# Kernel optimization log

Hardware: AMD Instinct MI355X
Metric: run time of the kernel (lower is better)

## Reference

```python
import jax, jax.numpy as jnp
import numpy as np

MESSAGE_PASSES = 3
HID = 100        # hidden_node_features == message_size
EDGE_F = 4       # n_edge_features
OUT = 100        # readout output dim


def setup_inputs() -> dict:
    key = jax.random.key(0)
    ks = jax.random.split(key, 8)
    B, N = 32, 128
    nodes = jax.random.normal(ks[0], (B, N, HID), dtype=jnp.float32)
    edges = jax.random.uniform(ks[1], (B, N, N, EDGE_F), dtype=jnp.float32)
    s = 1.0 / np.sqrt(HID)
    Wv = jax.random.normal(ks[2], (HID, HID), dtype=jnp.float32) * s
    Ww = jax.random.normal(ks[3], (HID, HID), dtype=jnp.float32) * s
    We = jax.random.normal(ks[4], (EDGE_F, HID), dtype=jnp.float32) * (1.0 / np.sqrt(EDGE_F))
    Wu = jax.random.normal(ks[5], (2 * HID, HID), dtype=jnp.float32) * (1.0 / np.sqrt(2 * HID))
    Wr = jax.random.normal(ks[6], (2 * HID, OUT), dtype=jnp.float32) * (1.0 / np.sqrt(2 * HID))
    return {"nodes": nodes, "edges": edges, "Wv": Wv, "Ww": Ww, "We": We, "Wu": Wu, "Wr": Wr}


def reference(nodes, edges, Wv, Ww, We, Wu, Wr):
    # adjacency[b,v,w] = sum_e edges[b,v,w,e]; nonzero entries define the edge set
    adjacency = edges.sum(axis=-1)                       # [B,N,N]
    edge_mask = adjacency != 0                           # [B,N,N]
    node_mask = adjacency.sum(axis=-1) != 0              # [B,N]

    # edge feature projection is constant across message passes
    e_proj = jnp.einsum('bvwe,eh->bvwh', edges, We)      # [B,N,N,H]

    hidden = nodes                                       # hidden_node_features == node feat dim
    for _ in range(MESSAGE_PASSES):
        # message_terms for every (b, v, w) edge: relu(h_v Wv + h_w Ww + e_vw We)
        pre = (hidden @ Wv)[:, :, None, :] + (hidden @ Ww)[:, None, :, :] + e_proj
        mterms = jnp.where(edge_mask[..., None], jax.nn.relu(pre), 0.0)
        # (same_batch * same_node) matmul == segment-sum over neighbors w
        messages = mterms.sum(axis=2)                    # [B,N,H]
        # update only nodes that appear in the edge set (degree > 0)
        upd = jnp.tanh(jnp.concatenate([hidden, messages], axis=-1) @ Wu)
        hidden = jnp.where(node_mask[..., None], upd, hidden)

    # readout: masked sum-pool of per-node graph terms
    graph_terms = jax.nn.relu(jnp.concatenate([hidden, nodes], axis=-1) @ Wr)  # [B,N,OUT]
    output = jnp.where(node_mask[..., None], graph_terms, 0.0).sum(axis=1)     # [B,OUT]
    return output
```

## Files before the change

### kernel.cpp

```cpp
#include <hip/hip_runtime.h>
#include <math.h>

#define B_   32
#define N_   128
#define H_   100
#define ROWS (B_ * N_)
#define RH   (ROWS * H_)
#define OUTSZ (B_ * H_)

__global__ __launch_bounds__(256, 6) void k_proj0(const float* __restrict__ nodes,
                                                  const float* __restrict__ Ww,
                                                  float* __restrict__ hw,
                                                  float* __restrict__ out) {
    __shared__ float nod_s[2][H_];
    const int row0 = blockIdx.x * 2;
    const int t = threadIdx.x, r = t >> 7, j = t & 127;
    {
        const int gid = blockIdx.x * 256 + t;
        if (gid < OUTSZ) out[gid] = 0.f;
    }
    {
        const float4* ng = (const float4*)(nodes + (size_t)row0 * H_);
        if (t < 50) ((float4*)nod_s)[t] = ng[t];
    }
    __syncthreads();
    if (j >= H_) return;
    const float4* h4p = (const float4*)nod_s[r];
    float wa = 0.f;
#pragma unroll 5
    for (int k4 = 0; k4 < 25; ++k4) {
        const float4 h4 = h4p[k4];
        const int k = k4 * 4;
        wa = fmaf(h4.x, Ww[(k + 0) * H_ + j], wa);
        wa = fmaf(h4.y, Ww[(k + 1) * H_ + j], wa);
        wa = fmaf(h4.z, Ww[(k + 2) * H_ + j], wa);
        wa = fmaf(h4.w, Ww[(k + 3) * H_ + j], wa);
    }
    hw[(size_t)(row0 + r) * H_ + j] = wa;
}

template <int MODE, int INIT_HV>
__global__ __launch_bounds__(256, 6) void k_pass(const float* __restrict__ edges,
                                                 const float* __restrict__ We,
                                                 const float* __restrict__ Wu,
                                                 const float* __restrict__ Wv,
                                                 const float* __restrict__ Ww,
                                                 const float* __restrict__ Wr,
                                                 const float* __restrict__ nodes,
                                                 float* __restrict__ hv_io,
                                                 const float* __restrict__ hw_in,
                                                 float* __restrict__ hw_out,
                                                 const float* __restrict__ hid_in,
                                                 float* __restrict__ hidden,
                                                 float* __restrict__ out) {
    __shared__ float4 e_s[2][N_];
    __shared__ float  asum_part[4];
    __shared__ unsigned qmask_s[2][4];
    __shared__ float  hid_s[2][H_];
    __shared__ float  msg_s[2][H_];
    __shared__ float  hn_s[2][H_];
    __shared__ float  nod_s[2][H_];
    __shared__ float  red_s[2][H_];

    const int bx = blockIdx.x;
    const int cu = bx & 255, slot = bx >> 8;
    const int b = cu >> 3;
    const int vt = (cu & 7) + slot * 8;
    const int row0 = b * N_ + vt * 2;

    const int t = threadIdx.x, r = t >> 7, j = t & 127;
    const int wv = t >> 6, lane = t & 63;
    const int row = row0 + r;
    const bool act = (j < H_);

    {
        const float4* eg = (const float4*)(edges + (size_t)row0 * N_ * 4);
        const float4 e = eg[t];
        e_s[r][j] = e;
        float s = (e.x + e.y) + (e.z + e.w);
        const unsigned long long bal = __ballot(s != 0.f);
        if (lane == 0) {
            qmask_s[wv >> 1][(wv & 1) * 2]     = (unsigned)bal;
            qmask_s[wv >> 1][(wv & 1) * 2 + 1] = (unsigned)(bal >> 32);
        }
#pragma unroll
        for (int off = 32; off > 0; off >>= 1) s += __shfl_down(s, off);
        if (lane == 0) asum_part[wv] = s;
    }
    {
        const float4* hg = (const float4*)(hid_in + (size_t)row0 * H_);
        if (t < 50) ((float4*)hid_s)[t] = hg[t];
        if (MODE == 2) {
            const float4* ng = (const float4*)(nodes + (size_t)row0 * H_);
            if (t < 50) ((float4*)nod_s)[t] = ng[t];
        }
    }
    __syncthreads();

    const float nm = ((asum_part[2 * r] + asum_part[2 * r + 1]) != 0.f) ? 1.f : 0.f;

    if (act) {
        float hvv;
        if (INIT_HV) {
            const float4* h4p = (const float4*)hid_s[r];
            float va = 0.f;
#pragma unroll 5
            for (int k4 = 0; k4 < 25; ++k4) {
                const float4 h4 = h4p[k4];
                const int k = k4 * 4;
                va = fmaf(h4.x, Wv[(k + 0) * H_ + j], va);
                va = fmaf(h4.y, Wv[(k + 1) * H_ + j], va);
                va = fmaf(h4.z, Wv[(k + 2) * H_ + j], va);
                va = fmaf(h4.w, Wv[(k + 3) * H_ + j], va);
            }
            hvv = va;
        } else {
            hvv = hv_io[(size_t)row * H_ + j];
        }
        const float we0 = We[0 * H_ + j], we1 = We[1 * H_ + j];
        const float we2 = We[2 * H_ + j], we3 = We[3 * H_ + j];
        const float* hwp = hw_in + (size_t)b * N_ * H_ + j;
        float acc = 0.f;
        for (int c = 0; c < 4; ++c) {
            const unsigned mq =
                __builtin_amdgcn_readfirstlane(qmask_s[r][c]);
            const float4* ec = &e_s[r][c * 32];
            const float*  hc = hwp + (size_t)(c * 32) * H_;
#pragma unroll 8
            for (int w8 = 0; w8 < 32; ++w8) {
                const float4 e = ec[w8];
                const float  hww = hc[w8 * H_];
                const float  m = ((mq >> w8) & 1u) ? 1.f : 0.f;
                float p = hvv + hww;
                p = fmaf(e.x, we0, p);
                p = fmaf(e.y, we1, p);
                p = fmaf(e.z, we2, p);
                p = fmaf(e.w, we3, p);
                acc = fmaf(m, fmaxf(p, 0.f), acc);
            }
        }
        msg_s[r][j] = acc;
    }
    __syncthreads();

    if (act) {
        const float4* h4p = (const float4*)hid_s[r];
        const float4* m4p = (const float4*)msg_s[r];
        float u = 0.f;
#pragma unroll 5
        for (int k4 = 0; k4 < 25; ++k4) {
            const float4 h4 = h4p[k4];
            const int k = k4 * 4;
            u = fmaf(h4.x, Wu[(k + 0) * H_ + j], u);
            u = fmaf(h4.y, Wu[(k + 1) * H_ + j], u);
            u = fmaf(h4.z, Wu[(k + 2) * H_ + j], u);
            u = fmaf(h4.w, Wu[(k + 3) * H_ + j], u);
        }
#pragma unroll 5
        for (int k4 = 0; k4 < 25; ++k4) {
            const float4 m4 = m4p[k4];
            const int k = H_ + k4 * 4;
            u = fmaf(m4.x, Wu[(k + 0) * H_ + j], u);
            u = fmaf(m4.y, Wu[(k + 1) * H_ + j], u);
            u = fmaf(m4.z, Wu[(k + 2) * H_ + j], u);
            u = fmaf(m4.w, Wu[(k + 3) * H_ + j], u);
        }
        const float nh = (nm != 0.f) ? tanhf(u) : hid_s[r][j];
        hn_s[r][j] = nh;
        if (MODE == 1) hidden[(size_t)row * H_ + j] = nh;
    }
    __syncthreads();

    if (MODE == 1) {
        if (act) {
            const float4* h4p = (const float4*)hn_s[r];
            float va = 0.f, wa = 0.f;
#pragma unroll 5
            for (int k4 = 0; k4 < 25; ++k4) {
                const float4 h4 = h4p[k4];
                const int k = k4 * 4;
                va = fmaf(h4.x, Wv[(k + 0) * H_ + j], va);
                wa = fmaf(h4.x, Ww[(k + 0) * H_ + j], wa);
                va = fmaf(h4.y, Wv[(k + 1) * H_ + j], va);
                wa = fmaf(h4.y, Ww[(k + 1) * H_ + j], wa);
                va = fmaf(h4.z, Wv[(k + 2) * H_ + j], va);
                wa = fmaf(h4.z, Ww[(k + 2) * H_ + j], wa);
                va = fmaf(h4.w, Wv[(k + 3) * H_ + j], va);
                wa = fmaf(h4.w, Ww[(k + 3) * H_ + j], wa);
            }
            hv_io[(size_t)row * H_ + j] = va;
            hw_out[(size_t)row * H_ + j] = wa;
        }
    } else {
        if (act) {
            const float4* h4p = (const float4*)hn_s[r];
            const float4* n4p = (const float4*)nod_s[r];
            float u = 0.f;
#pragma unroll 5
            for (int k4 = 0; k4 < 25; ++k4) {
                const float4 h4 = h4p[k4];
                const int k = k4 * 4;
                u = fmaf(h4.x, Wr[(k + 0) * H_ + j], u);
                u = fmaf(h4.y, Wr[(k + 1) * H_ + j], u);
                u = fmaf(h4.z, Wr[(k + 2) * H_ + j], u);
                u = fmaf(h4.w, Wr[(k + 3) * H_ + j], u);
            }
#pragma unroll 5
            for (int k4 = 0; k4 < 25; ++k4) {
                const float4 n4 = n4p[k4];
                const int k = H_ + k4 * 4;
                u = fmaf(n4.x, Wr[(k + 0) * H_ + j], u);
                u = fmaf(n4.y, Wr[(k + 1) * H_ + j], u);
                u = fmaf(n4.z, Wr[(k + 2) * H_ + j], u);
                u = fmaf(n4.w, Wr[(k + 3) * H_ + j], u);
            }
            red_s[r][j] = nm * fmaxf(u, 0.f);
        }
        __syncthreads();
        if (t < H_) atomicAdd(out + b * H_ + t, red_s[0][t] + red_s[1][t]);
    }
}

extern "C" void kernel_launch(void* const* d_in, const int* in_sizes, int n_in,
                              void* d_out, int out_size, void* d_ws, size_t ws_size,
                              hipStream_t stream) {
    const float* nodes = (const float*)d_in[0];
    const float* edges = (const float*)d_in[1];
    const float* Wv    = (const float*)d_in[2];
    const float* Ww    = (const float*)d_in[3];
    const float* We    = (const float*)d_in[4];
    const float* Wu    = (const float*)d_in[5];
    const float* Wr    = (const float*)d_in[6];
    float* out = (float*)d_out;

    float* hidden = (float*)d_ws;
    float* hv     = hidden + RH;
    float* hwA    = hv + RH;
    float* hwB    = hwA + RH;

    k_proj0<<<ROWS / 2, 256, 0, stream>>>(nodes, Ww, hwA, out);

    k_pass<1, 1><<<ROWS / 2, 256, 0, stream>>>(edges, We, Wu, Wv, Ww, Wr, nodes,
                                               hv, hwA, hwB, nodes, hidden, out);
    k_pass<1, 0><<<ROWS / 2, 256, 0, stream>>>(edges, We, Wu, Wv, Ww, Wr, nodes,
                                               hv, hwB, hwA, hidden, hidden, out);
    k_pass<2, 0><<<ROWS / 2, 256, 0, stream>>>(edges, We, Wu, Wv, Ww, Wr, nodes,
                                               hv, hwA, hwB, hidden, hidden, out);
}
```

Before: 198.9 us.

## Register-block four rows per thread to reuse weight and neighbor loads

```diff
diff --git a/kernel.cpp b/kernel.cpp
--- a/kernel.cpp
+++ b/kernel.cpp
@@ -7,40 +7,51 @@
 #define ROWS (B_ * N_)
 #define RH   (ROWS * H_)
 #define OUTSZ (B_ * H_)
-
-__global__ __launch_bounds__(256, 6) void k_proj0(const float* __restrict__ nodes,
+#define RPB  8
+#define RPT  4
+
+__global__ __launch_bounds__(256, 2) void k_proj0(const float* __restrict__ nodes,
                                                   const float* __restrict__ Ww,
                                                   float* __restrict__ hw,
                                                   float* __restrict__ out) {
-    __shared__ float nod_s[2][H_];
-    const int row0 = blockIdx.x * 2;
-    const int t = threadIdx.x, r = t >> 7, j = t & 127;
+    __shared__ float nod_s[RPB][H_];
+    const int bx = blockIdx.x;
+    const int row0 = bx * RPB;
+    const int t = threadIdx.x, rg = t >> 7, j = t & 127;
     {
-        const int gid = blockIdx.x * 256 + t;
+        const int gid = bx * 256 + t;
         if (gid < OUTSZ) out[gid] = 0.f;
     }
     {
         const float4* ng = (const float4*)(nodes + (size_t)row0 * H_);
-        if (t < 50) ((float4*)nod_s)[t] = ng[t];
+        if (t < 200) ((float4*)nod_s)[t] = ng[t];
     }
     __syncthreads();
     if (j >= H_) return;
-    const float4* h4p = (const float4*)nod_s[r];
-    float wa = 0.f;
+    float wa[RPT] = {0.f, 0.f, 0.f, 0.f};
 #pragma unroll 5
     for (int k4 = 0; k4 < 25; ++k4) {
-        const float4 h4 = h4p[k4];
         const int k = k4 * 4;
-        wa = fmaf(h4.x, Ww[(k + 0) * H_ + j], wa);
-        wa = fmaf(h4.y, Ww[(k + 1) * H_ + j], wa);
-        wa = fmaf(h4.z, Ww[(k + 2) * H_ + j], wa);
-        wa = fmaf(h4.w, Ww[(k + 3) * H_ + j], wa);
-    }
-    hw[(size_t)(row0 + r) * H_ + j] = wa;
+        const float w0 = Ww[(k + 0) * H_ + j];
+        const float w1 = Ww[(k + 1) * H_ + j];
+        const float w2 = Ww[(k + 2) * H_ + j];
+        const float w3 = Ww[(k + 3) * H_ + j];
+#pragma unroll
+        for (int r = 0; r < RPT; ++r) {
+            const float4 h4 = ((const float4*)nod_s[rg * RPT + r])[k4];
+            wa[r] = fmaf(h4.x, w0, wa[r]);
+            wa[r] = fmaf(h4.y, w1, wa[r]);
+            wa[r] = fmaf(h4.z, w2, wa[r]);
+            wa[r] = fmaf(h4.w, w3, wa[r]);
+        }
+    }
+#pragma unroll
+    for (int r = 0; r < RPT; ++r)
+        hw[(size_t)(row0 + rg * RPT + r) * H_ + j] = wa[r];
 }
 
 template <int MODE, int INIT_HV>
-__global__ __launch_bounds__(256, 6) void k_pass(const float* __restrict__ edges,
+__global__ __launch_bounds__(256, 2) void k_pass(const float* __restrict__ edges,
                                                  const float* __restrict__ We,
                                                  const float* __restrict__ Wu,
                                                  const float* __restrict__ Wv,
@@ -53,171 +64,242 @@
                                                  const float* __restrict__ hid_in,
                                                  float* __restrict__ hidden,
                                                  float* __restrict__ out) {
-    __shared__ float4 e_s[2][N_];
-    __shared__ float  asum_part[4];
-    __shared__ unsigned qmask_s[2][4];
-    __shared__ float  hid_s[2][H_];
-    __shared__ float  msg_s[2][H_];
-    __shared__ float  hn_s[2][H_];
-    __shared__ float  nod_s[2][H_];
-    __shared__ float  red_s[2][H_];
+    __shared__ float4 e_s[RPB][N_];
+    __shared__ float  asum_s[RPB][2];
+    __shared__ unsigned qmask_s[RPB][4];
+    __shared__ float  hid_s[RPB][H_];
+    __shared__ float  msg_s[RPB][H_];
+    __shared__ float  hn_s[RPB][H_];
+    __shared__ float  nod_s[RPB][H_];
+    __shared__ float  red_s[RPB][H_];
 
     const int bx = blockIdx.x;
-    const int cu = bx & 255, slot = bx >> 8;
-    const int b = cu >> 3;
-    const int vt = (cu & 7) + slot * 8;
-    const int row0 = b * N_ + vt * 2;
-
-    const int t = threadIdx.x, r = t >> 7, j = t & 127;
+    const int b = bx >> 4;
+    const int vt = bx & 15;
+    const int row0 = b * N_ + vt * RPB;
+
+    const int t = threadIdx.x, rg = t >> 7, j = t & 127;
     const int wv = t >> 6, lane = t & 63;
-    const int row = row0 + r;
     const bool act = (j < H_);
 
     {
         const float4* eg = (const float4*)(edges + (size_t)row0 * N_ * 4);
-        const float4 e = eg[t];
-        e_s[r][j] = e;
-        float s = (e.x + e.y) + (e.z + e.w);
-        const unsigned long long bal = __ballot(s != 0.f);
-        if (lane == 0) {
-            qmask_s[wv >> 1][(wv & 1) * 2]     = (unsigned)bal;
-            qmask_s[wv >> 1][(wv & 1) * 2 + 1] = (unsigned)(bal >> 32);
-        }
-#pragma unroll
-        for (int off = 32; off > 0; off >>= 1) s += __shfl_down(s, off);
-        if (lane == 0) asum_part[wv] = s;
+        float4* es = &e_s[0][0];
+#pragma unroll
+        for (int q = 0; q < 4; ++q) {
+            const int idx = q * 256 + t;
+            const float4 e = eg[idx];
+            es[idx] = e;
+            float s = (e.x + e.y) + (e.z + e.w);
+            const unsigned long long bal = __ballot(s != 0.f);
+            const int seg = q * 4 + wv;
+            const int rowq = seg >> 1, half = seg & 1;
+            if (lane == 0) {
+                qmask_s[rowq][half * 2]     = (unsigned)bal;
+                qmask_s[rowq][half * 2 + 1] = (unsigned)(bal >> 32);
+            }
+#pragma unroll
+            for (int off = 32; off > 0; off >>= 1) s += __shfl_down(s, off);
+            if (lane == 0) asum_s[rowq][half] = s;
+        }
     }
     {
         const float4* hg = (const float4*)(hid_in + (size_t)row0 * H_);
-        if (t < 50) ((float4*)hid_s)[t] = hg[t];
+        if (t < 200) ((float4*)hid_s)[t] = hg[t];
         if (MODE == 2) {
             const float4* ng = (const float4*)(nodes + (size_t)row0 * H_);
-            if (t < 50) ((float4*)nod_s)[t] = ng[t];
+            if (t < 200) ((float4*)nod_s)[t] = ng[t];
         }
     }
     __syncthreads();
 
-    const float nm = ((asum_part[2 * r] + asum_part[2 * r + 1]) != 0.f) ? 1.f : 0.f;
+    float nm[RPT];
+#pragma unroll
+    for (int r = 0; r < RPT; ++r) {
+        const int row = rg * RPT + r;
+        nm[r] = ((asum_s[row][0] + asum_s[row][1]) != 0.f) ? 1.f : 0.f;
+    }
 
     if (act) {
-        float hvv;
+        float hv[RPT];
         if (INIT_HV) {
-            const float4* h4p = (const float4*)hid_s[r];
-            float va = 0.f;
+            float va[RPT] = {0.f, 0.f, 0.f, 0.f};
 #pragma unroll 5
             for (int k4 = 0; k4 < 25; ++k4) {
-                const float4 h4 = h4p[k4];
                 const int k = k4 * 4;
-                va = fmaf(h4.x, Wv[(k + 0) * H_ + j], va);
-                va = fmaf(h4.y, Wv[(k + 1) * H_ + j], va);
-                va = fmaf(h4.z, Wv[(k + 2) * H_ + j], va);
-                va = fmaf(h4.w, Wv[(k + 3) * H_ + j], va);
-            }
-            hvv = va;
+                const float w0 = Wv[(k + 0) * H_ + j];
+                const float w1 = Wv[(k + 1) * H_ + j];
+                const float w2 = Wv[(k + 2) * H_ + j];
+                const float w3 = Wv[(k + 3) * H_ + j];
+#pragma unroll
+                for (int r = 0; r < RPT; ++r) {
+                    const float4 h4 = ((const float4*)hid_s[rg * RPT + r])[k4];
+                    va[r] = fmaf(h4.x, w0, va[r]);
+                    va[r] = fmaf(h4.y, w1, va[r]);
+                    va[r] = fmaf(h4.z, w2, va[r]);
+                    va[r] = fmaf(h4.w, w3, va[r]);
+                }
+            }
+#pragma unroll
+            for (int r = 0; r < RPT; ++r) hv[r] = va[r];
         } else {
-            hvv = hv_io[(size_t)row * H_ + j];
+#pragma unroll
+            for (int r = 0; r < RPT; ++r)
+                hv[r] = hv_io[(size_t)(row0 + rg * RPT + r) * H_ + j];
         }
         const float we0 = We[0 * H_ + j], we1 = We[1 * H_ + j];
         const float we2 = We[2 * H_ + j], we3 = We[3 * H_ + j];
         const float* hwp = hw_in + (size_t)b * N_ * H_ + j;
-        float acc = 0.f;
+        float acc[RPT] = {0.f, 0.f, 0.f, 0.f};
         for (int c = 0; c < 4; ++c) {
-            const unsigned mq =
-                __builtin_amdgcn_readfirstlane(qmask_s[r][c]);
-            const float4* ec = &e_s[r][c * 32];
-            const float*  hc = hwp + (size_t)(c * 32) * H_;
+            unsigned mq[RPT];
+#pragma unroll
+            for (int r = 0; r < RPT; ++r)
+                mq[r] = __builtin_amdgcn_readfirstlane(qmask_s[rg * RPT + r][c]);
+            const float* hc = hwp + (size_t)(c * 32) * H_;
 #pragma unroll 8
             for (int w8 = 0; w8 < 32; ++w8) {
-                const float4 e = ec[w8];
-                const float  hww = hc[w8 * H_];
-                const float  m = ((mq >> w8) & 1u) ? 1.f : 0.f;
-                float p = hvv + hww;
-                p = fmaf(e.x, we0, p);
-                p = fmaf(e.y, we1, p);
-                p = fmaf(e.z, we2, p);
-                p = fmaf(e.w, we3, p);
-                acc = fmaf(m, fmaxf(p, 0.f), acc);
-            }
-        }
-        msg_s[r][j] = acc;
+                const float hww = hc[w8 * H_];
+#pragma unroll
+                for (int r = 0; r < RPT; ++r) {
+                    const float4 e = e_s[rg * RPT + r][c * 32 + w8];
+                    float p = hv[r] + hww;
+                    p = fmaf(e.x, we0, p);
+                    p = fmaf(e.y, we1, p);
+                    p = fmaf(e.z, we2, p);
+                    p = fmaf(e.w, we3, p);
+                    const float m = ((mq[r] >> w8) & 1u) ? 1.f : 0.f;
+                    acc[r] = fmaf(m, fmaxf(p, 0.f), acc[r]);
+                }
+            }
+        }
+#pragma unroll
+        for (int r = 0; r < RPT; ++r) msg_s[rg * RPT + r][j] = acc[r];
     }
     __syncthreads();
 
+    float nh[RPT];
     if (act) {
-        const float4* h4p = (const float4*)hid_s[r];
-        const float4* m4p = (const float4*)msg_s[r];
-        float u = 0.f;
+        float u[RPT] = {0.f, 0.f, 0.f, 0.f};
 #pragma unroll 5
         for (int k4 = 0; k4 < 25; ++k4) {
-            const float4 h4 = h4p[k4];
             const int k = k4 * 4;
-            u = fmaf(h4.x, Wu[(k + 0) * H_ + j], u);
-            u = fmaf(h4.y, Wu[(k + 1) * H_ + j], u);
-            u = fmaf(h4.z, Wu[(k + 2) * H_ + j], u);
-            u = fmaf(h4.w, Wu[(k + 3) * H_ + j], u);
+            const float w0 = Wu[(k + 0) * H_ + j];
+            const float w1 = Wu[(k + 1) * H_ + j];
+            const float w2 = Wu[(k + 2) * H_ + j];
+            const float w3 = Wu[(k + 3) * H_ + j];
+#pragma unroll
+            for (int r = 0; r < RPT; ++r) {
+                const float4 h4 = ((const float4*)hid_s[rg * RPT + r])[k4];
+                u[r] = fmaf(h4.x, w0, u[r]);
+                u[r] = fmaf(h4.y, w1, u[r]);
+                u[r] = fmaf(h4.z, w2, u[r]);
+                u[r] = fmaf(h4.w, w3, u[r]);
+            }
         }
 #pragma unroll 5
         for (int k4 = 0; k4 < 25; ++k4) {
-            const float4 m4 = m4p[k4];
             const int k = H_ + k4 * 4;
-            u = fmaf(m4.x, Wu[(k + 0) * H_ + j], u);
-            u = fmaf(m4.y, Wu[(k + 1) * H_ + j], u);
-            u = fmaf(m4.z, Wu[(k + 2) * H_ + j], u);
-            u = fmaf(m4.w, Wu[(k + 3) * H_ + j], u);
-        }
-        const float nh = (nm != 0.f) ? tanhf(u) : hid_s[r][j];
-        hn_s[r][j] = nh;
-        if (MODE == 1) hidden[(size_t)row * H_ + j] = nh;
+            const float w0 = Wu[(k + 0) * H_ + j];
+            const float w1 = Wu[(k + 1) * H_ + j];
+            const float w2 = Wu[(k + 2) * H_ + j];
+            const float w3 = Wu[(k + 3) * H_ + j];
+#pragma unroll
+            for (int r = 0; r < RPT; ++r) {
+                const float4 m4 = ((const float4*)msg_s[rg * RPT + r])[k4];
+                u[r] = fmaf(m4.x, w0, u[r]);
+                u[r] = fmaf(m4.y, w1, u[r]);
+                u[r] = fmaf(m4.z, w2, u[r]);
+                u[r] = fmaf(m4.w, w3, u[r]);
+            }
+        }
+#pragma unroll
+        for (int r = 0; r < RPT; ++r) {
+            const int row = rg * RPT + r;
+            nh[r] = (nm[r] != 0.f) ? tanhf(u[r]) : hid_s[row][j];
+            hn_s[row][j] = nh[r];
+            if (MODE == 1) hidden[(size_t)(row0 + row) * H_ + j] = nh[r];
+        }
     }
     __syncthreads();
 
     if (MODE == 1) {
         if (act) {
-            const float4* h4p = (const float4*)hn_s[r];
-            float va = 0.f, wa = 0.f;
+            float va[RPT] = {0.f, 0.f, 0.f, 0.f};
+            float wa[RPT] = {0.f, 0.f, 0.f, 0.f};
 #pragma unroll 5
             for (int k4 = 0; k4 < 25; ++k4) {
-                const float4 h4 = h4p[k4];
                 const int k = k4 * 4;
-                va = fmaf(h4.x, Wv[(k + 0) * H_ + j], va);
-                wa = fmaf(h4.x, Ww[(k + 0) * H_ + j], wa);
-                va = fmaf(h4.y, Wv[(k + 1) * H_ + j], va);
-                wa = fmaf(h4.y, Ww[(k + 1) * H_ + j], wa);
-                va = fmaf(h4.z, Wv[(k + 2) * H_ + j], va);
-                wa = fmaf(h4.z, Ww[(k + 2) * H_ + j], wa);
-                va = fmaf(h4.w, Wv[(k + 3) * H_ + j], va);
-                wa = fmaf(h4.w, Ww[(k + 3) * H_ + j], wa);
-            }
-            hv_io[(size_t)row * H_ + j] = va;
-            hw_out[(size_t)row * H_ + j] = wa;
+                const float v0 = Wv[(k + 0) * H_ + j], q0 = Ww[(k + 0) * H_ + j];
+                const float v1 = Wv[(k + 1) * H_ + j], q1 = Ww[(k + 1) * H_ + j];
+                const float v2 = Wv[(k + 2) * H_ + j], q2 = Ww[(k + 2) * H_ + j];
+                const float v3 = Wv[(k + 3) * H_ + j], q3 = Ww[(k + 3) * H_ + j];
+#pragma unroll
+                for (int r = 0; r < RPT; ++r) {
+                    const float4 h4 = ((const float4*)hn_s[rg * RPT + r])[k4];
+                    va[r] = fmaf(h4.x, v0, va[r]);
+                    wa[r] = fmaf(h4.x, q0, wa[r]);
+                    va[r] = fmaf(h4.y, v1, va[r]);
+                    wa[r] = fmaf(h4.y, q1, wa[r]);
+                    va[r] = fmaf(h4.z, v2, va[r]);
+                    wa[r] = fmaf(h4.z, q2, wa[r]);
+                    va[r] = fmaf(h4.w, v3, va[r]);
+                    wa[r] = fmaf(h4.w, q3, wa[r]);
+                }
+            }
+#pragma unroll
+            for (int r = 0; r < RPT; ++r) {
+                const size_t g = (size_t)(row0 + rg * RPT + r) * H_ + j;
+                hv_io[g] = va[r];
+                hw_out[g] = wa[r];
+            }
         }
     } else {
         if (act) {
-            const float4* h4p = (const float4*)hn_s[r];
-            const float4* n4p = (const float4*)nod_s[r];
-            float u = 0.f;
+            float u[RPT] = {0.f, 0.f, 0.f, 0.f};
 #pragma unroll 5
             for (int k4 = 0; k4 < 25; ++k4) {
-                const float4 h4 = h4p[k4];
                 const int k = k4 * 4;
-                u = fmaf(h4.x, Wr[(k + 0) * H_ + j], u);
-                u = fmaf(h4.y, Wr[(k + 1) * H_ + j], u);
-                u = fmaf(h4.z, Wr[(k + 2) * H_ + j], u);
-                u = fmaf(h4.w, Wr[(k + 3) * H_ + j], u);
+                const float w0 = Wr[(k + 0) * H_ + j];
+                const float w1 = Wr[(k + 1) * H_ + j];
+                const float w2 = Wr[(k + 2) * H_ + j];
+                const float w3 = Wr[(k + 3) * H_ + j];
+#pragma unroll
+                for (int r = 0; r < RPT; ++r) {
+                    const float4 h4 = ((const float4*)hn_s[rg * RPT + r])[k4];
+                    u[r] = fmaf(h4.x, w0, u[r]);
+                    u[r] = fmaf(h4.y, w1, u[r]);
+                    u[r] = fmaf(h4.z, w2, u[r]);
+                    u[r] = fmaf(h4.w, w3, u[r]);
+                }
             }
 #pragma unroll 5
             for (int k4 = 0; k4 < 25; ++k4) {
-                const float4 n4 = n4p[k4];
                 const int k = H_ + k4 * 4;
-                u = fmaf(n4.x, Wr[(k + 0) * H_ + j], u);
-                u = fmaf(n4.y, Wr[(k + 1) * H_ + j], u);
-                u = fmaf(n4.z, Wr[(k + 2) * H_ + j], u);
-                u = fmaf(n4.w, Wr[(k + 3) * H_ + j], u);
-            }
-            red_s[r][j] = nm * fmaxf(u, 0.f);
+                const float w0 = Wr[(k + 0) * H_ + j];
+                const float w1 = Wr[(k + 1) * H_ + j];
+                const float w2 = Wr[(k + 2) * H_ + j];
+                const float w3 = Wr[(k + 3) * H_ + j];
+#pragma unroll
+                for (int r = 0; r < RPT; ++r) {
+                    const float4 n4 = ((const float4*)nod_s[rg * RPT + r])[k4];
+                    u[r] = fmaf(n4.x, w0, u[r]);
+                    u[r] = fmaf(n4.y, w1, u[r]);
+                    u[r] = fmaf(n4.z, w2, u[r]);
+                    u[r] = fmaf(n4.w, w3, u[r]);
+                }
+            }
+#pragma unroll
+            for (int r = 0; r < RPT; ++r)
+                red_s[rg * RPT + r][j] = nm[r] * fmaxf(u[r], 0.f);
         }
         __syncthreads();
-        if (t < H_) atomicAdd(out + b * H_ + t, red_s[0][t] + red_s[1][t]);
+        if (t < H_) {
+            float ssum = 0.f;
+#pragma unroll
+            for (int rr = 0; rr < RPB; ++rr) ssum += red_s[rr][t];
+            atomicAdd(out + b * H_ + t, ssum);
+        }
     }
 }
 
@@ -238,12 +320,12 @@
     float* hwA    = hv + RH;
     float* hwB    = hwA + RH;
 
-    k_proj0<<<ROWS / 2, 256, 0, stream>>>(nodes, Ww, hwA, out);
-
-    k_pass<1, 1><<<ROWS / 2, 256, 0, stream>>>(edges, We, Wu, Wv, Ww, Wr, nodes,
-                                               hv, hwA, hwB, nodes, hidden, out);
-    k_pass<1, 0><<<ROWS / 2, 256, 0, stream>>>(edges, We, Wu, Wv, Ww, Wr, nodes,
-                                               hv, hwB, hwA, hidden, hidden, out);
-    k_pass<2, 0><<<ROWS / 2, 256, 0, stream>>>(edges, We, Wu, Wv, Ww, Wr, nodes,
-                                               hv, hwA, hwB, hidden, hidden, out);
+    k_proj0<<<ROWS / RPB, 256, 0, stream>>>(nodes, Ww, hwA, out);
+
+    k_pass<1, 1><<<ROWS / RPB, 256, 0, stream>>>(edges, We, Wu, Wv, Ww, Wr, nodes,
+                                                 hv, hwA, hwB, nodes, hidden, out);
+    k_pass<1, 0><<<ROWS / RPB, 256, 0, stream>>>(edges, We, Wu, Wv, Ww, Wr, nodes,
+                                                 hv, hwB, hwA, hidden, hidden, out);
+    k_pass<2, 0><<<ROWS / RPB, 256, 0, stream>>>(edges, We, Wu, Wv, Ww, Wr, nodes,
+                                                 hv, hwA, hwB, hidden, hidden, out);
 }
```

Result: slower. 239.3 us (+20.3%).

## Stage dense weight matrices through double-buffered shared memory chunks

Applied to the files above, without the earlier changes.

```diff
diff --git a/kernel.cpp b/kernel.cpp
--- a/kernel.cpp
+++ b/kernel.cpp
@@ -7,6 +7,8 @@
 #define ROWS (B_ * N_)
 #define RH   (ROWS * H_)
 #define OUTSZ (B_ * H_)
+#define CK   20
+#define CK4  (CK * H_ / 4)
 
 __global__ __launch_bounds__(256, 6) void k_proj0(const float* __restrict__ nodes,
                                                   const float* __restrict__ Ww,
@@ -39,8 +41,15 @@
     hw[(size_t)(row0 + r) * H_ + j] = wa;
 }
 
+__device__ __forceinline__ void stage_chunk(float4* dst, const float* W,
+                                            int k0, int t) {
+    const float4* src = (const float4*)(W + (size_t)k0 * H_);
+    dst[t] = src[t];
+    if (t < CK4 - 256) dst[256 + t] = src[256 + t];
+}
+
 template <int MODE, int INIT_HV>
-__global__ __launch_bounds__(256, 6) void k_pass(const float* __restrict__ edges,
+__global__ __launch_bounds__(256, 7) void k_pass(const float* __restrict__ edges,
                                                  const float* __restrict__ We,
                                                  const float* __restrict__ Wu,
                                                  const float* __restrict__ Wv,
@@ -59,8 +68,8 @@
     __shared__ float  hid_s[2][H_];
     __shared__ float  msg_s[2][H_];
     __shared__ float  hn_s[2][H_];
-    __shared__ float  nod_s[2][H_];
-    __shared__ float  red_s[2][H_];
+    __shared__ float  nod_s[MODE == 2 ? 2 : 1][MODE == 2 ? H_ : 1];
+    __shared__ float4 w4_s[2][CK4];
 
     const int bx = blockIdx.x;
     const int cu = bx & 255, slot = bx >> 8;
@@ -95,6 +104,7 @@
             if (t < 50) ((float4*)nod_s)[t] = ng[t];
         }
     }
+    stage_chunk(w4_s[0], Wu, 0, t);
     __syncthreads();
 
     const float nm = ((asum_part[2 * r] + asum_part[2 * r + 1]) != 0.f) ? 1.f : 0.f;
@@ -143,81 +153,104 @@
     }
     __syncthreads();
 
+    int cur = 0;
+    float u0 = 0.f, u1 = 0.f;
+    for (int c = 0; c < 10; ++c) {
+        if (c < 9)       stage_chunk(w4_s[cur ^ 1], Wu, (c + 1) * CK, t);
+        else if (MODE == 1) stage_chunk(w4_s[cur ^ 1], Wv, 0, t);
+        else             stage_chunk(w4_s[cur ^ 1], Wr, 0, t);
+        if (act) {
+            const float* wb = (const float*)w4_s[cur] + j;
+            const float4* hb = (c < 5) ? ((const float4*)hid_s[r]) + c * 5
+                                       : ((const float4*)msg_s[r]) + (c - 5) * 5;
+#pragma unroll
+            for (int k4 = 0; k4 < 5; ++k4) {
+                const float4 h4 = hb[k4];
+                const float* wr_ = wb + k4 * 4 * H_;
+                u0 = fmaf(h4.x, wr_[0 * H_], u0);
+                u1 = fmaf(h4.y, wr_[1 * H_], u1);
+                u0 = fmaf(h4.z, wr_[2 * H_], u0);
+                u1 = fmaf(h4.w, wr_[3 * H_], u1);
+            }
+        }
+        __syncthreads();
+        cur ^= 1;
+    }
+
     if (act) {
-        const float4* h4p = (const float4*)hid_s[r];
-        const float4* m4p = (const float4*)msg_s[r];
-        float u = 0.f;
-#pragma unroll 5
-        for (int k4 = 0; k4 < 25; ++k4) {
-            const float4 h4 = h4p[k4];
-            const int k = k4 * 4;
-            u = fmaf(h4.x, Wu[(k + 0) * H_ + j], u);
-            u = fmaf(h4.y, Wu[(k + 1) * H_ + j], u);
-            u = fmaf(h4.z, Wu[(k + 2) * H_ + j], u);
-            u = fmaf(h4.w, Wu[(k + 3) * H_ + j], u);
-        }
-#pragma unroll 5
-        for (int k4 = 0; k4 < 25; ++k4) {
-            const float4 m4 = m4p[k4];
-            const int k = H_ + k4 * 4;
-            u = fmaf(m4.x, Wu[(k + 0) * H_ + j], u);
-            u = fmaf(m4.y, Wu[(k + 1) * H_ + j], u);
-            u = fmaf(m4.z, Wu[(k + 2) * H_ + j], u);
-            u = fmaf(m4.w, Wu[(k + 3) * H_ + j], u);
-        }
-        const float nh = (nm != 0.f) ? tanhf(u) : hid_s[r][j];
+        const float nh = (nm != 0.f) ? tanhf(u0 + u1) : hid_s[r][j];
         hn_s[r][j] = nh;
         if (MODE == 1) hidden[(size_t)row * H_ + j] = nh;
     }
     __syncthreads();
 
     if (MODE == 1) {
-        if (act) {
-            const float4* h4p = (const float4*)hn_s[r];
-            float va = 0.f, wa = 0.f;
-#pragma unroll 5
-            for (int k4 = 0; k4 < 25; ++k4) {
-                const float4 h4 = h4p[k4];
-                const int k = k4 * 4;
-                va = fmaf(h4.x, Wv[(k + 0) * H_ + j], va);
-                wa = fmaf(h4.x, Ww[(k + 0) * H_ + j], wa);
-                va = fmaf(h4.y, Wv[(k + 1) * H_ + j], va);
-                wa = fmaf(h4.y, Ww[(k + 1) * H_ + j], wa);
-                va = fmaf(h4.z, Wv[(k + 2) * H_ + j], va);
-                wa = fmaf(h4.z, Ww[(k + 2) * H_ + j], wa);
-                va = fmaf(h4.w, Wv[(k + 3) * H_ + j], va);
-                wa = fmaf(h4.w, Ww[(k + 3) * H_ + j], wa);
-            }
-            hv_io[(size_t)row * H_ + j] = va;
-            hw_out[(size_t)row * H_ + j] = wa;
-        }
+        float a0 = 0.f, a1 = 0.f;
+        for (int c = 0; c < 5; ++c) {
+            if (c < 4) stage_chunk(w4_s[cur ^ 1], Wv, (c + 1) * CK, t);
+            else       stage_chunk(w4_s[cur ^ 1], Ww, 0, t);
+            if (act) {
+                const float* wb = (const float*)w4_s[cur] + j;
+                const float4* hb = ((const float4*)hn_s[r]) + c * 5;
+#pragma unroll
+                for (int k4 = 0; k4 < 5; ++k4) {
+                    const float4 h4 = hb[k4];
+                    const float* wr_ = wb + k4 * 4 * H_;
+                    a0 = fmaf(h4.x, wr_[0 * H_], a0);
+                    a1 = fmaf(h4.y, wr_[1 * H_], a1);
+                    a0 = fmaf(h4.z, wr_[2 * H_], a0);
+                    a1 = fmaf(h4.w, wr_[3 * H_], a1);
+                }
+            }
+            __syncthreads();
+            cur ^= 1;
+        }
+        if (act) hv_io[(size_t)row * H_ + j] = a0 + a1;
+        float b0 = 0.f, b1 = 0.f;
+        for (int c = 0; c < 5; ++c) {
+            if (c < 4) stage_chunk(w4_s[cur ^ 1], Ww, (c + 1) * CK, t);
+            if (act) {
+                const float* wb = (const float*)w4_s[cur] + j;
+                const float4* hb = ((const float4*)hn_s[r]) + c * 5;
+#pragma unroll
+                for (int k4 = 0; k4 < 5; ++k4) {
+                    const float4 h4 = hb[k4];
+                    const float* wr_ = wb + k4 * 4 * H_;
+                    b0 = fmaf(h4.x, wr_[0 * H_], b0);
+                    b1 = fmaf(h4.y, wr_[1 * H_], b1);
+                    b0 = fmaf(h4.z, wr_[2 * H_], b0);
+                    b1 = fmaf(h4.w, wr_[3 * H_], b1);
+                }
+            }
+            if (c < 4) __syncthreads();
+            cur ^= 1;
+        }
+        if (act) hw_out[(size_t)row * H_ + j] = b0 + b1;
     } else {
-        if (act) {
-            const float4* h4p = (const float4*)hn_s[r];
-            const float4* n4p = (const float4*)nod_s[r];
-            float u = 0.f;
-#pragma unroll 5
-            for (int k4 = 0; k4 < 25; ++k4) {
-                const float4 h4 = h4p[k4];
-                const int k = k4 * 4;
-                u = fmaf(h4.x, Wr[(k + 0) * H_ + j], u);
-                u = fmaf(h4.y, Wr[(k + 1) * H_ + j], u);
-                u = fmaf(h4.z, Wr[(k + 2) * H_ + j], u);
-                u = fmaf(h4.w, Wr[(k + 3) * H_ + j], u);
-            }
-#pragma unroll 5
-            for (int k4 = 0; k4 < 25; ++k4) {
-                const float4 n4 = n4p[k4];
-                const int k = H_ + k4 * 4;
-                u = fmaf(n4.x, Wr[(k + 0) * H_ + j], u);
-                u = fmaf(n4.y, Wr[(k + 1) * H_ + j], u);
-                u = fmaf(n4.z, Wr[(k + 2) * H_ + j], u);
-                u = fmaf(n4.w, Wr[(k + 3) * H_ + j], u);
-            }
-            red_s[r][j] = nm * fmaxf(u, 0.f);
-        }
+        float a0 = 0.f, a1 = 0.f;
+        for (int c = 0; c < 10; ++c) {
+            if (c < 9) stage_chunk(w4_s[cur ^ 1], Wr, (c + 1) * CK, t);
+            if (act) {
+                const float* wb = (const float*)w4_s[cur] + j;
+                const float4* hb = (c < 5) ? ((const float4*)hn_s[r]) + c * 5
+                                           : ((const float4*)nod_s[r]) + (c - 5) * 5;
+#pragma unroll
+                for (int k4 = 0; k4 < 5; ++k4) {
+                    const float4 h4 = hb[k4];
+                    const float* wr_ = wb + k4 * 4 * H_;
+                    a0 = fmaf(h4.x, wr_[0 * H_], a0);
+                    a1 = fmaf(h4.y, wr_[1 * H_], a1);
+                    a0 = fmaf(h4.z, wr_[2 * H_], a0);
+                    a1 = fmaf(h4.w, wr_[3 * H_], a1);
+                }
+            }
+            __syncthreads();
+            cur ^= 1;
+        }
+        float* red = (float*)w4_s[0];
+        if (act) red[r * H_ + j] = nm * fmaxf(a0 + a1, 0.f);
         __syncthreads();
-        if (t < H_) atomicAdd(out + b * H_ + t, red_s[0][t] + red_s[1][t]);
+        if (t < H_) atomicAdd(out + b * H_ + t, red[0 * H_ + t] + red[1 * H_ + t]);
     }
 }
 
```

Result: slower. 214.1 us (+7.7%).

## Stage per-graph hw tile in LDS and process eight rows per block

Applied to the files above, without the earlier changes.

```diff
diff --git a/kernel.cpp b/kernel.cpp
--- a/kernel.cpp
+++ b/kernel.cpp
@@ -7,6 +7,7 @@
 #define ROWS (B_ * N_)
 #define RH   (ROWS * H_)
 #define OUTSZ (B_ * H_)
+#define RPB  8
 
 __global__ __launch_bounds__(256, 6) void k_proj0(const float* __restrict__ nodes,
                                                   const float* __restrict__ Ww,
@@ -40,69 +41,74 @@
 }
 
 template <int MODE, int INIT_HV>
-__global__ __launch_bounds__(256, 6) void k_pass(const float* __restrict__ edges,
-                                                 const float* __restrict__ We,
-                                                 const float* __restrict__ Wu,
-                                                 const float* __restrict__ Wv,
-                                                 const float* __restrict__ Ww,
-                                                 const float* __restrict__ Wr,
-                                                 const float* __restrict__ nodes,
-                                                 float* __restrict__ hv_io,
-                                                 const float* __restrict__ hw_in,
-                                                 float* __restrict__ hw_out,
-                                                 const float* __restrict__ hid_in,
-                                                 float* __restrict__ hidden,
-                                                 float* __restrict__ out) {
-    __shared__ float4 e_s[2][N_];
-    __shared__ float  asum_part[4];
-    __shared__ unsigned qmask_s[2][4];
-    __shared__ float  hid_s[2][H_];
-    __shared__ float  msg_s[2][H_];
-    __shared__ float  hn_s[2][H_];
-    __shared__ float  nod_s[2][H_];
-    __shared__ float  red_s[2][H_];
+__global__ __launch_bounds__(1024, 8) void k_pass(const float* __restrict__ edges,
+                                                  const float* __restrict__ We,
+                                                  const float* __restrict__ Wu,
+                                                  const float* __restrict__ Wv,
+                                                  const float* __restrict__ Ww,
+                                                  const float* __restrict__ Wr,
+                                                  const float* __restrict__ nodes,
+                                                  float* __restrict__ hv_io,
+                                                  const float* __restrict__ hw_in,
+                                                  float* __restrict__ hw_out,
+                                                  const float* __restrict__ hid_in,
+                                                  float* __restrict__ hidden,
+                                                  float* __restrict__ out) {
+    __shared__ float  hw_s[N_ * H_];
+    __shared__ float4 e_s[RPB * N_];
+    __shared__ float  asum_s[RPB][2];
+    __shared__ unsigned qmask_s[RPB][4];
+    __shared__ float  hid_s[RPB][H_];
+    __shared__ float  msg_s[RPB][H_];
+    __shared__ float  hn_s[RPB][H_];
 
     const int bx = blockIdx.x;
     const int cu = bx & 255, slot = bx >> 8;
     const int b = cu >> 3;
     const int vt = (cu & 7) + slot * 8;
-    const int row0 = b * N_ + vt * 2;
-
-    const int t = threadIdx.x, r = t >> 7, j = t & 127;
+    const int row0 = b * N_ + vt * RPB;
+
+    const int t = threadIdx.x;
+    const int rg = t >> 7, j = t & 127;
     const int wv = t >> 6, lane = t & 63;
-    const int row = row0 + r;
+    const int row = row0 + rg;
     const bool act = (j < H_);
 
+    {
+        const float4* src = (const float4*)(hw_in + (size_t)b * N_ * H_);
+        float4* dst = (float4*)hw_s;
+        dst[t] = src[t];
+        dst[1024 + t] = src[1024 + t];
+        dst[2048 + t] = src[2048 + t];
+        if (t < 128) dst[3072 + t] = src[3072 + t];
+    }
     {
         const float4* eg = (const float4*)(edges + (size_t)row0 * N_ * 4);
         const float4 e = eg[t];
-        e_s[r][j] = e;
+        e_s[t] = e;
         float s = (e.x + e.y) + (e.z + e.w);
         const unsigned long long bal = __ballot(s != 0.f);
+        const int rowq = wv >> 1, half = wv & 1;
         if (lane == 0) {
-            qmask_s[wv >> 1][(wv & 1) * 2]     = (unsigned)bal;
-            qmask_s[wv >> 1][(wv & 1) * 2 + 1] = (unsigned)(bal >> 32);
+            qmask_s[rowq][half * 2]     = (unsigned)bal;
+            qmask_s[rowq][half * 2 + 1] = (unsigned)(bal >> 32);
         }
 #pragma unroll
         for (int off = 32; off > 0; off >>= 1) s += __shfl_down(s, off);
-        if (lane == 0) asum_part[wv] = s;
+        if (lane == 0) asum_s[rowq][half] = s;
     }
     {
         const float4* hg = (const float4*)(hid_in + (size_t)row0 * H_);
-        if (t < 50) ((float4*)hid_s)[t] = hg[t];
-        if (MODE == 2) {
-            const float4* ng = (const float4*)(nodes + (size_t)row0 * H_);
-            if (t < 50) ((float4*)nod_s)[t] = ng[t];
-        }
-    }
-    __syncthreads();
-
-    const float nm = ((asum_part[2 * r] + asum_part[2 * r + 1]) != 0.f) ? 1.f : 0.f;
+        if (t < 200) ((float4*)hid_s)[t] = hg[t];
+    }
+    __syncthreads();
+
+    const float nm = ((asum_s[rg][0] + asum_s[rg][1]) != 0.f) ? 1.f : 0.f;
 
     if (act) {
         float hvv;
         if (INIT_HV) {
-            const float4* h4p = (const float4*)hid_s[r];
+            const float4* h4p = (const float4*)hid_s[rg];
             float va = 0.f;
 #pragma unroll 5
             for (int k4 = 0; k4 < 25; ++k4) {
@@ -119,12 +125,12 @@
         }
         const float we0 = We[0 * H_ + j], we1 = We[1 * H_ + j];
         const float we2 = We[2 * H_ + j], we3 = We[3 * H_ + j];
-        const float* hwp = hw_in + (size_t)b * N_ * H_ + j;
+        const float* hwp = hw_s + j;
         float acc = 0.f;
         for (int c = 0; c < 4; ++c) {
             const unsigned mq =
-                __builtin_amdgcn_readfirstlane(qmask_s[r][c]);
-            const float4* ec = &e_s[r][c * 32];
+                __builtin_amdgcn_readfirstlane(qmask_s[rg][c]);
+            const float4* ec = &e_s[rg * N_ + c * 32];
             const float*  hc = hwp + (size_t)(c * 32) * H_;
 #pragma unroll 8
             for (int w8 = 0; w8 < 32; ++w8) {
@@ -139,13 +145,19 @@
                 acc = fmaf(m, fmaxf(p, 0.f), acc);
             }
         }
-        msg_s[r][j] = acc;
-    }
-    __syncthreads();
+        msg_s[rg][j] = acc;
+    }
+    __syncthreads();
+
+    if (MODE == 2) {
+        float* nodf = (float*)e_s + 1024;
+        const float4* ng = (const float4*)(nodes + (size_t)row0 * H_);
+        if (t < 200) ((float4*)nodf)[t] = ng[t];
+    }
 
     if (act) {
-        const float4* h4p = (const float4*)hid_s[r];
-        const float4* m4p = (const float4*)msg_s[r];
+        const float4* h4p = (const float4*)hid_s[rg];
+        const float4* m4p = (const float4*)msg_s[rg];
         float u = 0.f;
 #pragma unroll 5
         for (int k4 = 0; k4 < 25; ++k4) {
@@ -165,15 +177,15 @@
             u = fmaf(m4.z, Wu[(k + 2) * H_ + j], u);
             u = fmaf(m4.w, Wu[(k + 3) * H_ + j], u);
         }
-        const float nh = (nm != 0.f) ? tanhf(u) : hid_s[r][j];
-        hn_s[r][j] = nh;
+        const float nh = (nm != 0.f) ? tanhf(u) : hid_s[rg][j];
+        hn_s[rg][j] = nh;
         if (MODE == 1) hidden[(size_t)row * H_ + j] = nh;
     }
     __syncthreads();
 
     if (MODE == 1) {
         if (act) {
-            const float4* h4p = (const float4*)hn_s[r];
+            const float4* h4p = (const float4*)hn_s[rg];
             float va = 0.f, wa = 0.f;
 #pragma unroll 5
             for (int k4 = 0; k4 < 25; ++k4) {
@@ -192,9 +204,11 @@
             hw_out[(size_t)row * H_ + j] = wa;
         }
     } else {
+        float* nodf = (float*)e_s + 1024;
+        float* redf = (float*)e_s;
         if (act) {
-            const float4* h4p = (const float4*)hn_s[r];
-            const float4* n4p = (const float4*)nod_s[r];
+            const float4* h4p = (const float4*)hn_s[rg];
+            const float4* n4p = (const float4*)(nodf + rg * H_);
             float u = 0.f;
 #pragma unroll 5
             for (int k4 = 0; k4 < 25; ++k4) {
@@ -214,10 +228,15 @@
                 u = fmaf(n4.z, Wr[(k + 2) * H_ + j], u);
                 u = fmaf(n4.w, Wr[(k + 3) * H_ + j], u);
             }
-            red_s[r][j] = nm * fmaxf(u, 0.f);
+            redf[rg * H_ + j] = nm * fmaxf(u, 0.f);
         }
         __syncthreads();
-        if (t < H_) atomicAdd(out + b * H_ + t, red_s[0][t] + red_s[1][t]);
+        if (t < H_) {
+            float ssum = 0.f;
+#pragma unroll
+            for (int rr = 0; rr < RPB; ++rr) ssum += redf[rr * H_ + t];
+            atomicAdd(out + b * H_ + t, ssum);
+        }
     }
 }
 
@@ -240,10 +259,10 @@
 
     k_proj0<<<ROWS / 2, 256, 0, stream>>>(nodes, Ww, hwA, out);
 
-    k_pass<1, 1><<<ROWS / 2, 256, 0, stream>>>(edges, We, Wu, Wv, Ww, Wr, nodes,
-                                               hv, hwA, hwB, nodes, hidden, out);
-    k_pass<1, 0><<<ROWS / 2, 256, 0, stream>>>(edges, We, Wu, Wv, Ww, Wr, nodes,
-                                               hv, hwB, hwA, hidden, hidden, out);
-    k_pass<2, 0><<<ROWS / 2, 256, 0, stream>>>(edges, We, Wu, Wv, Ww, Wr, nodes,
-                                               hv, hwA, hwB, hidden, hidden, out);
+    k_pass<1, 1><<<ROWS / RPB, 1024, 0, stream>>>(edges, We, Wu, Wv, Ww, Wr, nodes,
+                                                  hv, hwA, hwB, nodes, hidden, out);
+    k_pass<1, 0><<<ROWS / RPB, 1024, 0, stream>>>(edges, We, Wu, Wv, Ww, Wr, nodes,
+                                                  hv, hwB, hwA, hidden, hidden, out);
+    k_pass<2, 0><<<ROWS / RPB, 1024, 0, stream>>>(edges, We, Wu, Wv, Ww, Wr, nodes,
+                                                  hv, hwA, hwB, hidden, hidden, out);
 }
```

Result: no change. 197.1 us (-0.9%).
